# Performance work log

Hardware: AMD Instinct MI355X
Metric: run time of the kernel (lower is better)

Reference implementation:

```python
import jax, jax.numpy as jnp
import numpy as np
from jax import lax

B, D, C, K = 8192, 512, 1000, 8
EPS = 1e-8
TEMP = 0.2
NEG = -10000.0


def setup_inputs() -> dict:
    key = jax.random.key(0)
    ks = jax.random.split(key, 6)
    z = jax.random.normal(ks[0], (B, D), dtype=jnp.float32)
    n_exp = jax.random.randint(ks[1], (B,), 0, K, dtype=jnp.int32)
    s1 = 1.0 / np.sqrt(D)
    W1 = jax.random.normal(ks[2], (K, D, D), dtype=jnp.float32) * s1
    b1 = jax.random.normal(ks[3], (K, D), dtype=jnp.float32) * 0.01
    W2 = jax.random.normal(ks[4], (K, D, C), dtype=jnp.float32) * s1
    b2 = jax.random.normal(ks[5], (K, C), dtype=jnp.float32) * 0.01
    return {"z": z, "n_exp": n_exp, "W1": W1, "b1": b1, "W2": W2, "b2": b2}


def _gates_one(p, c, n):
    # p: [K,C] softmax probs for one sample; c: [K] confidences; n: scalar int
    pn = p / (jnp.linalg.norm(p, axis=-1, keepdims=True) + EPS)
    S = pn @ pn.T  # [K,K] pairwise cosine similarity
    sel0 = jnp.zeros((K,), dtype=bool).at[jnp.argmax(c)].set(True)

    def body(t, sel):
        # max cosine sim of each candidate to already-selected set
        max_sim = jnp.max(jnp.where(sel[None, :], S, -jnp.inf), axis=1)
        dist = jnp.where(sel, -jnp.inf, 1.0 - max_sim)
        new = sel.at[jnp.argmax(dist)].set(True)
        return jnp.where(t < n, new, sel)

    sel = lax.fori_loop(1, K, body, sel0)
    gate_logits = jnp.where(sel, c, NEG) / TEMP
    return jax.nn.softmax(gate_logits)


def reference(z, n_exp, W1, b1, W2, b2):
    # K expert MLPs, batched: [B,d] -> [B,K,C]
    h = jax.nn.relu(jnp.einsum('bd,kde->bke', z, W1) + b1[None])
    logits_all = jnp.einsum('bke,kec->bkc', h, W2) + b2[None]
    probs = jax.nn.softmax(logits_all, axis=-1)
    conf = jnp.max(probs, axis=-1)  # [B,K]
    gates = jax.vmap(_gates_one)(probs, conf, n_exp)  # [B,K]
    logits = jnp.einsum('bkc,bk->bc', logits_all, gates)
    return logits, gates
```

## Files before the change

kernel.cpp:

```cpp
#include <hip/hip_runtime.h>
#include <math.h>

#define B_SZ 8192
#define D_DIM 512
#define C_DIM 1000
#define C_PAD 1024
#define K_EXP 8
#define TEMP_INV 5.0f
#define EPS_N 1e-8f

typedef __attribute__((ext_vector_type(8))) short frag_ab;
typedef __attribute__((ext_vector_type(4))) float frag_cd;

__device__ __forceinline__ short f2bf(float f) {
    unsigned u = __builtin_bit_cast(unsigned, f);
    unsigned r = (u + 0x7fffu + ((u >> 16) & 1u)) >> 16;
    return (short)r;
}
__device__ __forceinline__ float bf2f(short s) {
    unsigned u = ((unsigned)(unsigned short)s) << 16;
    return __builtin_bit_cast(float, u);
}
__device__ __forceinline__ void split2(float v, short& s0, short& s1) {
    s0 = f2bf(v);
    s1 = f2bf(v - bf2f(s0));
}

__device__ __forceinline__ void gl_lds16(const short* g, short* l) {
    __builtin_amdgcn_global_load_lds(
        (const __attribute__((address_space(1))) unsigned int*)(const void*)g,
        (__attribute__((address_space(3))) unsigned int*)(void*)l,
        16, 0, 0);
}

__global__ __launch_bounds__(256) void prep_z(const float* __restrict__ z,
                                              short* __restrict__ p0, short* __restrict__ p1) {
    int idx = blockIdx.x * 256 + threadIdx.x;
    float v = z[idx];
    short a, b; split2(v, a, b);
    p0[idx] = a; p1[idx] = b;
}

__global__ __launch_bounds__(256) void prep_w1t(const float* __restrict__ W1,
                                                short* __restrict__ p0, short* __restrict__ p1) {
    __shared__ float t[32][33];
    const int k = blockIdx.z;
    const int d0 = blockIdx.x * 32;
    const int e0 = blockIdx.y * 32;
    const int tx = threadIdx.x & 31, ty = threadIdx.x >> 5;
    const float* src = W1 + ((size_t)k << 18);
#pragma unroll
    for (int r = 0; r < 4; r++) {
        int d = d0 + ty + 8 * r;
        t[ty + 8 * r][tx] = src[(size_t)d * 512 + e0 + tx];
    }
    __syncthreads();
#pragma unroll
    for (int r = 0; r < 4; r++) {
        int e = e0 + ty + 8 * r;
        int d = d0 + tx;
        float v = t[tx][ty + 8 * r];
        short a, b; split2(v, a, b);
        size_t o = ((size_t)k << 18) + (size_t)e * 512 + d;
        p0[o] = a; p1[o] = b;
    }
}

__global__ __launch_bounds__(256) void prep_w2t(const float* __restrict__ W2,
                                                short* __restrict__ p0, short* __restrict__ p1) {
    __shared__ float t[32][33];
    const int k = blockIdx.z;
    const int e0 = blockIdx.x * 32;
    const int c0 = blockIdx.y * 32;
    const int tx = threadIdx.x & 31, ty = threadIdx.x >> 5;
    const float* src = W2 + (size_t)k * (D_DIM * C_DIM);
#pragma unroll
    for (int r = 0; r < 4; r++) {
        int e = e0 + ty + 8 * r;
        int c = c0 + tx;
        t[ty + 8 * r][tx] = (c < C_DIM) ? src[(size_t)e * C_DIM + c] : 0.f;
    }
    __syncthreads();
#pragma unroll
    for (int r = 0; r < 4; r++) {
        int c = c0 + ty + 8 * r;
        int e = e0 + tx;
        float v = t[tx][ty + 8 * r];
        short a, b; split2(v, a, b);
        size_t o = (size_t)k * (C_PAD * D_DIM) + (size_t)c * 512 + e;
        p0[o] = a; p1[o] = b;
    }
}

__global__ __launch_bounds__(512, 2) void gemm_split(
    const short* __restrict__ A0, const short* __restrict__ A1, long long aBatch,
    const short* __restrict__ B0, const short* __restrict__ B1, long long bBatch,
    const float* __restrict__ bias, int biasBatch,
    float* __restrict__ Cf, long long cBatch, int ldc, int Nout,
    short* __restrict__ H0, short* __restrict__ H1, long long hBatch,
    int mt, int nt, int mode)
{
    const int lin = blockIdx.x;
    const int k = lin & 7;
    const int rem = lin >> 3;
    const int gm = (mt >= 2) ? 2 : 1;
    const int win = rem / (gm * nt);
    const int local = rem % (gm * nt);
    const int m0 = (win * gm + local / nt) * 256;
    const int n0 = (local % nt) * 256;

    const int tid = threadIdx.x;
    const int lane = tid & 63;
    const int wv = tid >> 6;
    const int wm = (wv & 1) * 128;
    const int wn = (wv >> 1) * 64;

    __shared__ short lds[65536];

    const short* gA0 = A0 + (size_t)k * aBatch + (size_t)m0 * 512;
    const short* gA1 = A1 + (size_t)k * aBatch + (size_t)m0 * 512;
    const short* gB0 = B0 + (size_t)k * bBatch + (size_t)n0 * 512;
    const short* gB1 = B1 + (size_t)k * bBatch + (size_t)n0 * 512;
    const short* ga[2] = {gA0, gA1};
    const short* gb[2] = {gB0, gB1};

    frag_cd acc[8][4];
#pragma unroll
    for (int i = 0; i < 8; i++)
#pragma unroll
        for (int j = 0; j < 4; j++)
            acc[i][j] = (frag_cd){0.f, 0.f, 0.f, 0.f};

    const int srow = tid >> 2;
    const int sc   = tid & 3;

#define STAGE(KK0, BUFO) do {                                                   \
    _Pragma("unroll")                                                           \
    for (int p = 0; p < 2; p++) {                                               \
        _Pragma("unroll")                                                       \
        for (int hh = 0; hh < 2; hh++) {                                        \
            int row = hh * 128 + srow;                                          \
            int gq = sc ^ ((row >> 1) & 3);                                     \
            gl_lds16(ga[p] + (size_t)row * 512 + (KK0) + gq * 8,                \
                     lds + (BUFO) + p * 8192 + row * 32 + sc * 8);              \
            gl_lds16(gb[p] + (size_t)row * 512 + (KK0) + gq * 8,                \
                     lds + 32768 + (BUFO) + p * 8192 + row * 32 + sc * 8);      \
        }                                                                       \
    }                                                                           \
} while (0)

    const int q = lane >> 4;
    const int rb = lane & 15;

    auto compute = [&](int bufo) {
        const short* bA = lds + bufo;
        const short* bB = lds + 32768 + bufo;
        frag_ab bfr[2][4];
#pragma unroll
        for (int p = 0; p < 2; p++)
#pragma unroll
            for (int j = 0; j < 4; j++) {
                int R = wn + j * 16 + rb;
                int slot = q ^ ((R >> 1) & 3);
                bfr[p][j] = *(const frag_ab*)(bB + p * 8192 + R * 32 + slot * 8);
            }
        __builtin_amdgcn_s_setprio(1);
#pragma unroll
        for (int i = 0; i < 8; i++) {
            int R = wm + i * 16 + rb;
            int slot = q ^ ((R >> 1) & 3);
            frag_ab a0 = *(const frag_ab*)(bA + R * 32 + slot * 8);
            frag_ab a1 = *(const frag_ab*)(bA + 8192 + R * 32 + slot * 8);
#pragma unroll
            for (int j = 0; j < 4; j++) {
                frag_cd c = acc[i][j];
                c = __builtin_amdgcn_mfma_f32_16x16x32_bf16(a0, bfr[0][j], c, 0, 0, 0);
                c = __builtin_amdgcn_mfma_f32_16x16x32_bf16(a0, bfr[1][j], c, 0, 0, 0);
                c = __builtin_amdgcn_mfma_f32_16x16x32_bf16(a1, bfr[0][j], c, 0, 0, 0);
                acc[i][j] = c;
            }
        }
        __builtin_amdgcn_s_setprio(0);
    };

    STAGE(0, 0);

    for (int t = 0; t < 15; t++) {
        STAGE((t + 1) * 32, ((t + 1) & 1) * 16384);
        asm volatile("s_waitcnt vmcnt(8)" ::: "memory");
        __builtin_amdgcn_s_barrier();
        __builtin_amdgcn_sched_barrier(0);
        compute((t & 1) * 16384);
        __builtin_amdgcn_sched_barrier(0);
        __builtin_amdgcn_s_barrier();
    }
    asm volatile("s_waitcnt vmcnt(0)" ::: "memory");
    __builtin_amdgcn_s_barrier();
    __builtin_amdgcn_sched_barrier(0);
    compute(16384);
#undef STAGE

    const int r0 = (lane >> 4) * 4;
    const int cc = lane & 15;
    if (mode == 0) {
        float* C = Cf + (size_t)k * cBatch;
        const float* bb = bias + (size_t)k * biasBatch;
#pragma unroll
        for (int i = 0; i < 8; i++) {
            int rowb = m0 + wm + i * 16 + r0;
#pragma unroll
            for (int j = 0; j < 4; j++) {
                int col = n0 + wn + j * 16 + cc;
                if (col < Nout) {
                    float b = bb[col];
#pragma unroll
                    for (int r = 0; r < 4; r++)
                        C[(size_t)(rowb + r) * ldc + col] = acc[i][j][r] + b;
                }
            }
        }
    } else {
        short* h0 = H0 + (size_t)k * hBatch;
        short* h1 = H1 + (size_t)k * hBatch;
        const float* bb = bias + (size_t)k * biasBatch;
#pragma unroll
        for (int i = 0; i < 8; i++) {
            int rowb = m0 + wm + i * 16 + r0;
#pragma unroll
            for (int j = 0; j < 4; j++) {
                int col = n0 + wn + j * 16 + cc;
                float b = bb[col];
#pragma unroll
                for (int r = 0; r < 4; r++) {
                    float v = fmaxf(acc[i][j][r] + b, 0.f);
                    short s0, s1; split2(v, s0, s1);
                    size_t o = (size_t)(rowb + r) * 512 + col;
                    h0[o] = s0; h1[o] = s1;
                }
            }
        }
    }
}

__global__ __launch_bounds__(256) void gate_combine(
    const float* __restrict__ L,
    const int* __restrict__ n_exp,
    float* __restrict__ out_logits,
    float* __restrict__ out_gates,
    int Bc)
{
    const int wv = threadIdx.x >> 6;
    const int lane = threadIdx.x & 63;
    const int b = blockIdx.x * 4 + wv;
    const size_t kcs = (size_t)Bc * C_DIM;
    const float* Lb = L + (size_t)b * C_DIM;

    __shared__ float Sm[4][64];
    __shared__ float Zm[4][8];

    float mx[K_EXP], Zs[K_EXP], dd[36];
#pragma unroll
    for (int k = 0; k < K_EXP; k++) { mx[k] = -INFINITY; Zs[k] = 0.f; }
#pragma unroll
    for (int p = 0; p < 36; p++) dd[p] = 0.f;

    for (int c = lane; c < C_DIM; c += 64) {
        float e[K_EXP];
#pragma unroll
        for (int k = 0; k < K_EXP; k++) {
            float l = Lb[(size_t)k * kcs + c];
            mx[k] = fmaxf(mx[k], l);
            e[k] = __expf(l);
            Zs[k] += e[k];
        }
        int idx = 0;
#pragma unroll
        for (int i = 0; i < K_EXP; i++)
#pragma unroll
            for (int j = i; j < K_EXP; j++) {
                dd[idx] = fmaf(e[i], e[j], dd[idx]);
                idx++;
            }
    }

#pragma unroll
    for (int off = 32; off > 0; off >>= 1) {
#pragma unroll
        for (int k = 0; k < K_EXP; k++) {
            mx[k] = fmaxf(mx[k], __shfl_xor(mx[k], off, 64));
            Zs[k] += __shfl_xor(Zs[k], off, 64);
        }
#pragma unroll
        for (int p = 0; p < 36; p++)
            dd[p] += __shfl_xor(dd[p], off, 64);
    }

    if (lane == 0) {
        int idx = 0;
#pragma unroll
        for (int i = 0; i < K_EXP; i++)
#pragma unroll
            for (int j = i; j < K_EXP; j++) {
                Sm[wv][i * 8 + j] = dd[idx];
                Sm[wv][j * 8 + i] = dd[idx];
                idx++;
            }
#pragma unroll
        for (int k = 0; k < K_EXP; k++) Zm[wv][k] = Zs[k];
    }

    const int ti = lane >> 3, tj = lane & 7;
    const float Zi = Zm[wv][ti], Zj = Zm[wv][tj];
    const float dij = Sm[wv][ti * 8 + tj];
    const float dii = Sm[wv][ti * 8 + ti];
    const float djj = Sm[wv][tj * 8 + tj];
    const float ni = sqrtf(dii) / Zi + EPS_N;
    const float nj = sqrtf(djj) / Zj + EPS_N;
    const float cosij = (dij / (Zi * Zj)) / (ni * nj);

    float conf[K_EXP];
#pragma unroll
    for (int k = 0; k < K_EXP; k++) conf[k] = __expf(mx[k]) / Zs[k];

    int i0 = 0; float bcf = conf[0];
#pragma unroll
    for (int k = 1; k < K_EXP; k++)
        if (conf[k] > bcf) { bcf = conf[k]; i0 = k; }
    unsigned sel = 1u << i0;
    const int n = n_exp[b];

    for (int t = 1; t < K_EXP; t++) {
        float v = ((sel >> tj) & 1u) ? cosij : -INFINITY;
        v = fmaxf(v, __shfl_xor(v, 1, 64));
        v = fmaxf(v, __shfl_xor(v, 2, 64));
        v = fmaxf(v, __shfl_xor(v, 4, 64));
        float dist = ((sel >> ti) & 1u) ? -INFINITY : 1.0f - v;
        float bv = dist; int bi = ti;
#pragma unroll
        for (int off = 8; off < 64; off <<= 1) {
            float ov = __shfl_xor(bv, off, 64);
            int oi = __shfl_xor(bi, off, 64);
            if (ov > bv || (ov == bv && oi < bi)) { bv = ov; bi = oi; }
        }
        if (t < n) sel |= 1u << bi;
    }

    float cmax = -INFINITY;
#pragma unroll
    for (int k = 0; k < K_EXP; k++)
        if ((sel >> k) & 1u) cmax = fmaxf(cmax, conf[k]);
    float g[K_EXP], gsum = 0.f;
#pragma unroll
    for (int k = 0; k < K_EXP; k++) {
        g[k] = ((sel >> k) & 1u) ? __expf((conf[k] - cmax) * TEMP_INV) : 0.f;
        gsum += g[k];
    }
    const float ginv = 1.0f / gsum;
#pragma unroll
    for (int k = 0; k < K_EXP; k++) g[k] *= ginv;

    if (lane == 0) {
        float4* og = (float4*)(out_gates + (size_t)b * K_EXP);
        og[0] = make_float4(g[0], g[1], g[2], g[3]);
        og[1] = make_float4(g[4], g[5], g[6], g[7]);
    }

    for (int c = lane; c < C_DIM; c += 64) {
        float o = 0.f;
#pragma unroll
        for (int k = 0; k < K_EXP; k++)
            o = fmaf(g[k], Lb[(size_t)k * kcs + c], o);
        out_logits[(size_t)b * C_DIM + c] = o;
    }
}

extern "C" void kernel_launch(void* const* d_in, const int* in_sizes, int n_in,
                              void* d_out, int out_size, void* d_ws, size_t ws_size,
                              hipStream_t stream) {
    const float* z     = (const float*)d_in[0];
    const int*   n_exp = (const int*)d_in[1];
    const float* W1    = (const float*)d_in[2];
    const float* b1    = (const float*)d_in[3];
    const float* W2    = (const float*)d_in[4];
    const float* b2    = (const float*)d_in[5];
    float* out_logits = (float*)d_out;
    float* out_gates  = (float*)d_out + (size_t)B_SZ * C_DIM;

    const size_t zP   = (size_t)B_SZ * D_DIM * 2;
    const size_t w1P  = (size_t)K_EXP * D_DIM * D_DIM * 2;
    const size_t w2P  = (size_t)K_EXP * C_PAD * D_DIM * 2;
    const size_t fixedBytes = 2 * (zP + w1P + w2P);

    int nch = 1;
    while (nch < 32 && fixedBytes + (size_t)(B_SZ / nch) * 48384 > ws_size) nch *= 2;
    const int Bc = B_SZ / nch;

    char* w = (char*)d_ws;
    short* zp[2];  zp[0]  = (short*)w; zp[1]  = (short*)(w + zP);  w += 2 * zP;
    short* w1t[2]; w1t[0] = (short*)w; w1t[1] = (short*)(w + w1P); w += 2 * w1P;
    short* w2t[2]; w2t[0] = (short*)w; w2t[1] = (short*)(w + w2P); w += 2 * w2P;
    const size_t hP = (size_t)K_EXP * Bc * D_DIM * 2;
    short* hp[2];  hp[0]  = (short*)w; hp[1]  = (short*)(w + hP);  w += 2 * hP;
    float* Lb = (float*)w;

    prep_z <<<dim3((B_SZ * D_DIM) / 256), 256, 0, stream>>>(z, zp[0], zp[1]);
    prep_w1t<<<dim3(16, 16, K_EXP), 256, 0, stream>>>(W1, w1t[0], w1t[1]);
    prep_w2t<<<dim3(16, 32, K_EXP), 256, 0, stream>>>(W2, w2t[0], w2t[1]);

    const int mt = Bc / 256;

    for (int ch = 0; ch < nch; ch++) {
        const int off = ch * Bc;
        const long long zoff = (long long)off * D_DIM;

        gemm_split<<<dim3(8 * mt * 2), 512, 0, stream>>>(
            zp[0] + zoff, zp[1] + zoff, 0LL,
            w1t[0], w1t[1], (long long)D_DIM * D_DIM,
            b1, D_DIM,
            nullptr, 0LL, 0, D_DIM,
            hp[0], hp[1], (long long)Bc * D_DIM,
            mt, 2, 1);

        gemm_split<<<dim3(8 * mt * 4), 512, 0, stream>>>(
            hp[0], hp[1], (long long)Bc * D_DIM,
            w2t[0], w2t[1], (long long)C_PAD * D_DIM,
            b2, C_DIM,
            Lb, (long long)Bc * C_DIM, C_DIM, C_DIM,
            nullptr, nullptr, 0LL,
            mt, 4, 0);

        gate_combine<<<dim3(Bc / 4), 256, 0, stream>>>(
            Lb, n_exp + off,
            out_logits + (size_t)off * C_DIM,
            out_gates + (size_t)off * K_EXP,
            Bc);
    }
}
```

Before: 493.5 us.

## Interleave global-to-LDS staging with MFMA quarters in GEMM k-loop

```diff
diff --git a/kernel.cpp b/kernel.cpp
--- a/kernel.cpp
+++ b/kernel.cpp
@@ -116,13 +116,13 @@
     const int wn = (wv >> 1) * 64;
 
     __shared__ short lds[65536];
-
-    const short* gA0 = A0 + (size_t)k * aBatch + (size_t)m0 * 512;
-    const short* gA1 = A1 + (size_t)k * aBatch + (size_t)m0 * 512;
-    const short* gB0 = B0 + (size_t)k * bBatch + (size_t)n0 * 512;
-    const short* gB1 = B1 + (size_t)k * bBatch + (size_t)n0 * 512;
-    const short* ga[2] = {gA0, gA1};
-    const short* gb[2] = {gB0, gB1};
+    short* ldsA = lds;
+    short* ldsB = lds + 32768;
+
+    const short* aP0 = A0 + (size_t)k * aBatch + (size_t)m0 * 512;
+    const short* aP1 = A1 + (size_t)k * aBatch + (size_t)m0 * 512;
+    const short* bP0 = B0 + (size_t)k * bBatch + (size_t)n0 * 512;
+    const short* bP1 = B1 + (size_t)k * bBatch + (size_t)n0 * 512;
 
     frag_cd acc[8][4];
 #pragma unroll
@@ -133,72 +133,106 @@
 
     const int srow = tid >> 2;
     const int sc   = tid & 3;
-
-#define STAGE(KK0, BUFO) do {                                                   \
+    const int q    = lane >> 4;
+    const int rb   = lane & 15;
+
+#define SROW_STAGE(gsrc, ldst, KK0) do {                                        \
     _Pragma("unroll")                                                           \
-    for (int p = 0; p < 2; p++) {                                               \
-        _Pragma("unroll")                                                       \
-        for (int hh = 0; hh < 2; hh++) {                                        \
-            int row = hh * 128 + srow;                                          \
-            int gq = sc ^ ((row >> 1) & 3);                                     \
-            gl_lds16(ga[p] + (size_t)row * 512 + (KK0) + gq * 8,                \
-                     lds + (BUFO) + p * 8192 + row * 32 + sc * 8);              \
-            gl_lds16(gb[p] + (size_t)row * 512 + (KK0) + gq * 8,                \
-                     lds + 32768 + (BUFO) + p * 8192 + row * 32 + sc * 8);      \
-        }                                                                       \
+    for (int hh = 0; hh < 2; hh++) {                                            \
+        int row = hh * 128 + srow;                                              \
+        int gq = sc ^ ((row >> 1) & 3);                                         \
+        gl_lds16((gsrc) + (size_t)row * 512 + (KK0) + gq * 8,                   \
+                 (ldst) + row * 32 + sc * 8);                                   \
     }                                                                           \
 } while (0)
 
-    const int q = lane >> 4;
-    const int rb = lane & 15;
-
-    auto compute = [&](int bufo) {
-        const short* bA = lds + bufo;
-        const short* bB = lds + 32768 + bufo;
-        frag_ab bfr[2][4];
-#pragma unroll
-        for (int p = 0; p < 2; p++)
+#define AREAD(P)                                                                \
+    frag_ab a0_[2], a1_[2];                                                     \
+    _Pragma("unroll")                                                           \
+    for (int ii = 0; ii < 2; ii++) {                                            \
+        int R = wm + ((P) * 2 + ii) * 16 + rb;                                  \
+        int slot = q ^ ((R >> 1) & 3);                                          \
+        a0_[ii] = *(const frag_ab*)(ldsA + bufc + R * 32 + slot * 8);           \
+        a1_[ii] = *(const frag_ab*)(ldsA + bufc + 8192 + R * 32 + slot * 8);    \
+    }
+
+#define QMFMA(P) do {                                                           \
+    __builtin_amdgcn_s_setprio(1);                                              \
+    _Pragma("unroll")                                                           \
+    for (int ii = 0; ii < 2; ii++)                                              \
+        _Pragma("unroll")                                                       \
+        for (int j = 0; j < 4; j++) {                                           \
+            frag_cd c = acc[(P) * 2 + ii][j];                                   \
+            c = __builtin_amdgcn_mfma_f32_16x16x32_bf16(a0_[ii], bfr0[j], c, 0, 0, 0); \
+            c = __builtin_amdgcn_mfma_f32_16x16x32_bf16(a0_[ii], bfr1[j], c, 0, 0, 0); \
+            c = __builtin_amdgcn_mfma_f32_16x16x32_bf16(a1_[ii], bfr0[j], c, 0, 0, 0); \
+            acc[(P) * 2 + ii][j] = c;                                           \
+        }                                                                       \
+    __builtin_amdgcn_s_setprio(0);                                              \
+} while (0)
+
+    SROW_STAGE(bP0, ldsB + 0,            0);
+    SROW_STAGE(bP1, ldsB + 8192,         0);
+    SROW_STAGE(aP0, ldsA + 0,            0);
+    SROW_STAGE(aP1, ldsA + 8192,         0);
+    SROW_STAGE(bP0, ldsB + 16384,        32);
+    SROW_STAGE(bP1, ldsB + 16384 + 8192, 32);
+    asm volatile("s_waitcnt vmcnt(4)" ::: "memory");
+    __builtin_amdgcn_s_barrier();
+
+    auto kstep = [&](int T, bool s01, bool s23, int vmn) __attribute__((always_inline)) {
+        const int bufc = (T & 1) * 16384;
+        const int nb1  = ((T + 1) & 1) * 16384;
+        const int kk1  = (T + 1) * 32;
+        const int kk2  = (T + 2) * 32;
+        frag_ab bfr0[4], bfr1[4];
+
+        {
 #pragma unroll
             for (int j = 0; j < 4; j++) {
                 int R = wn + j * 16 + rb;
                 int slot = q ^ ((R >> 1) & 3);
-                bfr[p][j] = *(const frag_ab*)(bB + p * 8192 + R * 32 + slot * 8);
+                bfr0[j] = *(const frag_ab*)(ldsB + bufc + R * 32 + slot * 8);
+                bfr1[j] = *(const frag_ab*)(ldsB + bufc + 8192 + R * 32 + slot * 8);
             }
-        __builtin_amdgcn_s_setprio(1);
-#pragma unroll
-        for (int i = 0; i < 8; i++) {
-            int R = wm + i * 16 + rb;
-            int slot = q ^ ((R >> 1) & 3);
-            frag_ab a0 = *(const frag_ab*)(bA + R * 32 + slot * 8);
-            frag_ab a1 = *(const frag_ab*)(bA + 8192 + R * 32 + slot * 8);
-#pragma unroll
-            for (int j = 0; j < 4; j++) {
-                frag_cd c = acc[i][j];
-                c = __builtin_amdgcn_mfma_f32_16x16x32_bf16(a0, bfr[0][j], c, 0, 0, 0);
-                c = __builtin_amdgcn_mfma_f32_16x16x32_bf16(a0, bfr[1][j], c, 0, 0, 0);
-                c = __builtin_amdgcn_mfma_f32_16x16x32_bf16(a1, bfr[0][j], c, 0, 0, 0);
-                acc[i][j] = c;
-            }
-        }
-        __builtin_amdgcn_s_setprio(0);
+            AREAD(0);
+            if (s01) SROW_STAGE(aP0, ldsA + nb1, kk1);
+            __builtin_amdgcn_s_barrier();
+            QMFMA(0);
+            __builtin_amdgcn_s_barrier();
+        }
+        {
+            AREAD(1);
+            if (s01) SROW_STAGE(aP1, ldsA + nb1 + 8192, kk1);
+            __builtin_amdgcn_s_barrier();
+            QMFMA(1);
+            __builtin_amdgcn_s_barrier();
+        }
+        {
+            AREAD(2);
+            if (s23) SROW_STAGE(bP0, ldsB + bufc, kk2);
+            __builtin_amdgcn_s_barrier();
+            QMFMA(2);
+            __builtin_amdgcn_s_barrier();
+        }
+        {
+            AREAD(3);
+            if (s23) SROW_STAGE(bP1, ldsB + bufc + 8192, kk2);
+            __builtin_amdgcn_s_barrier();
+            QMFMA(3);
+            if (vmn == 4)      asm volatile("s_waitcnt vmcnt(4)" ::: "memory");
+            else if (vmn == 0) asm volatile("s_waitcnt vmcnt(0)" ::: "memory");
+            __builtin_amdgcn_s_barrier();
+        }
     };
 
-    STAGE(0, 0);
-
-    for (int t = 0; t < 15; t++) {
-        STAGE((t + 1) * 32, ((t + 1) & 1) * 16384);
-        asm volatile("s_waitcnt vmcnt(8)" ::: "memory");
-        __builtin_amdgcn_s_barrier();
-        __builtin_amdgcn_sched_barrier(0);
-        compute((t & 1) * 16384);
-        __builtin_amdgcn_sched_barrier(0);
-        __builtin_amdgcn_s_barrier();
-    }
-    asm volatile("s_waitcnt vmcnt(0)" ::: "memory");
-    __builtin_amdgcn_s_barrier();
-    __builtin_amdgcn_sched_barrier(0);
-    compute(16384);
-#undef STAGE
+    for (int t = 0; t < 14; ++t) kstep(t, true, true, 4);
+    kstep(14, true, false, 0);
+    kstep(15, false, false, -1);
+
+#undef SROW_STAGE
+#undef AREAD
+#undef QMFMA
 
     const int r0 = (lane >> 4) * 4;
     const int cc = lane & 15;
```

Result: no change. 488.4 us (-1.0%).
